# Kernel tuning notes

Hardware: AMD Instinct MI355X
Metric: run time of the kernel (lower is better)

The kernel has to match this reference:

```python
import jax, jax.numpy as jnp
import numpy as np

K = 16

def _pairwise_distance(points):
    # points: (B, N, F) -> (B, N, N)
    r = jnp.sum(points * points, axis=2, keepdims=True)  # (B,N,1)
    m = jnp.einsum('bnf,bmf->bnm', points, points)
    return r - 2.0 * m + jnp.swapaxes(r, 1, 2) + 1e-5

def _block(points, features, W1, b1, W2, b2):
    D = _pairwise_distance(points)
    _, idx = jax.lax.top_k(-D, K + 1)          # (B,N,K+1)
    idx = idx[:, :, 1:]                          # drop self -> (B,N,K)
    neighbors = jax.vmap(lambda f, i: f[i])(features, idx)  # (B,N,K,C)
    center = jnp.broadcast_to(features[:, :, None, :], neighbors.shape)
    edge = jnp.concatenate([neighbors - center, center], axis=-1)  # (B,N,K,2C)
    h = jax.nn.gelu(edge @ W1 + b1, approximate=False)
    h = jax.nn.gelu(h @ W2 + b2, approximate=False)
    return jnp.mean(h, axis=2)  # (B,N,proj)

def setup_inputs() -> dict:
    key = jax.random.key(0)
    ks = jax.random.split(key, 8)
    B, N, C_in, P, F = 64, 512, 32, 64, 3
    s = lambda fan: 1.0 / np.sqrt(fan)
    return {
        'x': jax.random.normal(ks[0], (B, N, C_in), jnp.float32),
        'points': jax.random.normal(ks[1], (B, N, F), jnp.float32),
        'mask': jax.random.randint(ks[2], (B, N, 1), 0, 2).astype(jnp.int32),
        'W1_0': jax.random.normal(ks[3], (2 * C_in, 2 * P), jnp.float32) * s(2 * C_in),
        'b1_0': jnp.zeros((2 * P,), jnp.float32),
        'W2_0': jax.random.normal(ks[4], (2 * P, P), jnp.float32) * s(2 * P),
        'b2_0': jnp.zeros((P,), jnp.float32),
        'W1_1': jax.random.normal(ks[5], (2 * P, 2 * P), jnp.float32) * s(2 * P),
        'b1_1': jnp.zeros((2 * P,), jnp.float32),
        'W2_1': jax.random.normal(ks[6], (2 * P, P), jnp.float32) * s(2 * P),
        'b2_1': jnp.zeros((P,), jnp.float32),
    }

def reference(x, points, mask, W1_0, b1_0, W2_0, b2_0, W1_1, b1_1, W2_1, b2_1):
    mask_f = mask.astype(jnp.float32)
    coord_shift = 999.0 * (mask == 0).astype(jnp.float32)  # (B,N,1)
    feats = _block(coord_shift + points, x, W1_0, b1_0, W2_0, b2_0)
    feats = _block(coord_shift + feats, feats, W1_1, b1_1, W2_1, b2_1)
    return feats * mask_f
```

## Files before the change

kernel.cpp:

```cpp
#include <hip/hip_runtime.h>
#include <math.h>

#define BB 64
#define NN 512
#define KK 16

__device__ __forceinline__ float gelu32(float x) {
    return 0.5f * x * (1.0f + erff(x * 0.70710678118654752440f));
}

#define TAB_N 521
__device__ __forceinline__ double gelu64_tab(double x, const double2* s_tab) {
    double ax = fabs(x);
    if (ax >= 5.74) return x > 0.0 ? x : 0.0;
    double z = ax * 0.70710678118654752440;
    double u = z * 128.0;
    int i = (int)(u + 0.5);
    double zi = (double)i * (1.0 / 128.0);
    double d = z - zi;
    double2 t = s_tab[i];
    double poly = d * (1.0 + d * (-zi + d * ((2.0 * zi * zi - 1.0) * (1.0 / 3.0))));
    double er = t.x + t.y * poly;
    double s = (x > 0.0) ? er : -er;
    return 0.5 * x * (1.0 + s);
}

__global__ void build_tab(double2* __restrict__ g_tab) {
    for (int i = threadIdx.x; i < TAB_N; i += 256) {
        double z = (double)i * (1.0 / 128.0);
        double2 e;
        e.x = erf(z);
        e.y = 1.12837916709551257390 * exp(-z * z);
        g_tab[i] = e;
    }
}

#define SELECT_TOP17(d, lane, OUT_STMT)                                        \
    for (int it = 0; it <= KK; ++it) {                                         \
        double bd = d[0];                                                      \
        int bi = lane;                                                         \
        _Pragma("unroll")                                                      \
        for (int i = 1; i < 8; ++i) {                                          \
            int m = lane + 64 * i;                                             \
            if (d[i] < bd) { bd = d[i]; bi = m; }                              \
        }                                                                      \
        for (int off = 32; off > 0; off >>= 1) {                               \
            double od = __shfl_xor(bd, off, 64);                               \
            int    oi = __shfl_xor(bi, off, 64);                               \
            if (od < bd || (od == bd && oi < bi)) { bd = od; bi = oi; }        \
        }                                                                      \
        const int wl = bi & 63, wsl = bi >> 6;                                 \
        _Pragma("unroll")                                                      \
        for (int i = 0; i < 8; ++i)                                            \
            if (lane == wl && i == wsl) d[i] = 1e300;                          \
        if (it > 0 && lane == 0) { OUT_STMT; }                                 \
    }

__global__ __launch_bounds__(512) void knn1_uv1(const float* __restrict__ points,
                                                const int* __restrict__ mask,
                                                const float* __restrict__ x,
                                                const float* __restrict__ W1,
                                                int* __restrict__ idx_out,
                                                double* __restrict__ U1) {
    __shared__ double sbuf[3 * NN];
    const int tid = threadIdx.x;

    if (blockIdx.x < BB * NN / 8) {
        double (*pts)[NN] = (double (*)[NN])sbuf;
        const int b = blockIdx.x >> 6;
        const int n0 = (blockIdx.x & 63) * 8;
        const int w = tid >> 6, lane = tid & 63;

        for (int e = tid; e < NN; e += 512) {
            double sh = (mask[b * NN + e] == 0) ? 999.0 : 0.0;
            const float* p = points + ((size_t)b * NN + e) * 3;
            pts[0][e] = (double)p[0] + sh;
            pts[1][e] = (double)p[1] + sh;
            pts[2][e] = (double)p[2] + sh;
        }
        __syncthreads();

        const int n = n0 + w;
        if (mask[b * NN + n] == 0) return;
        const double q0 = pts[0][n], q1 = pts[1][n], q2 = pts[2][n];
        double d[8];
        #pragma unroll
        for (int i = 0; i < 8; ++i) {
            int m = lane + 64 * i;
            double d0 = q0 - pts[0][m], d1 = q1 - pts[1][m], d2 = q2 - pts[2][m];
            d[i] = d0 * d0 + d1 * d1 + d2 * d2;
        }

        int* orow = idx_out + (size_t)(b * NN + n) * KK;
        SELECT_TOP17(d, lane, orow[it - 1] = bi)
    } else {
        double (*xs)[32] = (double (*)[32])sbuf;
        const int row0 = (blockIdx.x - BB * NN / 8) * 8;
        if (tid < 256) xs[tid >> 5][tid & 31] = (double)x[(size_t)row0 * 32 + tid];
        __syncthreads();
        const int j = tid & 127;
        const int rr = tid >> 7;
        #pragma unroll
        for (int p = 0; p < 2; ++p) {
            const int r = p * 4 + rr;
            const int row = row0 + r;
            if (mask[row] != 0) {
                double acc = 0.0;
                #pragma unroll 4
                for (int c = 0; c < 32; ++c) acc += xs[r][c] * (double)W1[c * 128 + j];
                U1[(size_t)row * 128 + j] = acc;
            }
        }
    }
}

template<int UV>
__global__ __launch_bounds__(256, 2) void mlp1_f64(const float* __restrict__ x,
                                                   const int* __restrict__ idx,
                                                   const float* __restrict__ W1,
                                                   const float* __restrict__ b1,
                                                   const float* __restrict__ W2,
                                                   const float* __restrict__ b2,
                                                   const float* __restrict__ W1n,
                                                   const double2* __restrict__ g_tab,
                                                   const int* __restrict__ mask,
                                                   const double* __restrict__ U1,
                                                   double* __restrict__ feats_out,
                                                   double* __restrict__ rm,
                                                   double* __restrict__ Sq,
                                                   float* __restrict__ U2) {
    const int C = 32;
    __shared__ double2 s_tab[TAB_N];
    __shared__ double ctr[32];
    __shared__ double H1[KK][128];
    __shared__ double part[4][64];
    __shared__ float f_row[64];
    const int swz = ((blockIdx.x & 7) << 12) + (blockIdx.x >> 3);
    const int b = swz >> 9;
    const int bn = swz;
    const int tid = threadIdx.x;

    if (mask[bn] == 0) {
        if (tid == 0) { rm[bn] = 1e18; Sq[bn] = 0.0; }
        return;
    }

    for (int i = tid; i < TAB_N; i += 256) s_tab[i] = g_tab[i];
    if (tid < C) ctr[tid] = (double)x[(size_t)bn * C + tid];
    __syncthreads();

    if constexpr (UV) {
        const int j = tid & 127;
        const int kb = (tid >> 7) * 8;
        double tn = (double)b1[j];
        #pragma unroll 4
        for (int c = 0; c < C; ++c)
            tn += ctr[c] * ((double)W1[(C + c) * 128 + j] - (double)W1[c * 128 + j]);
        #pragma unroll
        for (int kk = 0; kk < 8; ++kk) {
            int m = idx[bn * KK + kb + kk];
            double v = U1[(size_t)(b * NN + m) * 128 + j] + tn;
            H1[kb + kk][j] = gelu64_tab(v, s_tab);
        }
    } else {
        __shared__ double edg[KK][32];
        for (int e = tid; e < KK * C; e += 256) {
            int k = e >> 5, c = e & 31;
            int m = idx[bn * KK + k];
            edg[k][c] = (double)x[((size_t)b * NN + m) * C + c] - ctr[c];
        }
        __syncthreads();
        const int j = tid & 127;
        const int kb = (tid >> 7) * 8;
        double cterm = (double)b1[j];
        #pragma unroll 2
        for (int c = 0; c < C; ++c) cterm += ctr[c] * (double)W1[(C + c) * 128 + j];
        double acc[8];
        #pragma unroll
        for (int kk = 0; kk < 8; ++kk) acc[kk] = cterm;
        #pragma unroll 2
        for (int c = 0; c < C; ++c) {
            double w = (double)W1[c * 128 + j];
            #pragma unroll
            for (int kk = 0; kk < 8; ++kk) acc[kk] += edg[kb + kk][c] * w;
        }
        #pragma unroll
        for (int kk = 0; kk < 8; ++kk) H1[kb + kk][j] = gelu64_tab(acc[kk], s_tab);
    }
    __syncthreads();

    {
        const int j = tid & 63;
        const int g = tid >> 6;
        const int kb = g * 4;
        double acc[4];
        #pragma unroll
        for (int kk = 0; kk < 4; ++kk) acc[kk] = (double)b2[j];
        #pragma unroll 4
        for (int c = 0; c < 128; ++c) {
            double w = (double)W2[c * 64 + j];
            #pragma unroll
            for (int kk = 0; kk < 4; ++kk) acc[kk] += H1[kb + kk][c] * w;
        }
        double s = 0.0;
        #pragma unroll
        for (int kk = 0; kk < 4; ++kk) s += gelu64_tab(acc[kk], s_tab);
        part[g][j] = s;
    }
    __syncthreads();

    if (tid < 64) {
        double s = (part[0][tid] + part[1][tid] + part[2][tid] + part[3][tid]) * 0.0625;
        feats_out[(size_t)bn * 64 + tid] = s;
        f_row[tid] = (float)s;
        double s2 = s * s, s1 = s;
        for (int off = 32; off > 0; off >>= 1) {
            s2 += __shfl_xor(s2, off, 64);
            s1 += __shfl_xor(s1, off, 64);
        }
        if (tid == 0) { rm[bn] = s2; Sq[bn] = s1; }
    }
    if constexpr (UV) {
        __syncthreads();
        if (tid < 128) {
            float acc = 0.0f;
            #pragma unroll 4
            for (int c = 0; c < 64; ++c) acc += f_row[c] * W1n[c * 128 + tid];
            U2[(size_t)bn * 128 + tid] = acc;
        }
    }
}

__global__ __launch_bounds__(512) void knn2(const double* __restrict__ feats,
                                            const int* __restrict__ mask,
                                            const double* __restrict__ rm,
                                            const double* __restrict__ Sq,
                                            int* __restrict__ idx_out) {
    __shared__ double tileT[64][65];
    __shared__ double qsh[8][64];
    __shared__ double qrn[8], qSq[8];
    const int bid = ((blockIdx.x & 7) << 9) + (blockIdx.x >> 3);
    const int b = bid >> 6;
    const int n0 = (bid & 63) * 8;
    const int tid = threadIdx.x;
    const int w = tid >> 6, lane = tid & 63;
    const int n = n0 + w;
    const int qm = mask[b * NN + n];

    {
        qsh[w][lane] = feats[(size_t)(b * NN + n) * 64 + lane];
        if (lane == 0) { qrn[w] = rm[b * NN + n]; qSq[w] = Sq[b * NN + n]; }
    }
    __syncthreads();

    double d[8];
    #pragma unroll
    for (int t = 0; t < 8; ++t) {
        #pragma unroll
        for (int i = 0; i < 8; ++i) {
            int e = tid + 512 * i;
            int f = e & 63, c = e >> 6;
            tileT[f][c] = feats[(size_t)(b * NN + t * 64 + c) * 64 + f];
        }
        __syncthreads();
        if (qm) {
            int m = t * 64 + lane;
            double sh_m = (mask[b * NN + m] == 0) ? 999.0 : 0.0;
            double a0 = 0.0, a1 = 0.0, a2 = 0.0, a3 = 0.0;
            for (int f = 0; f < 64; f += 4) {
                a0 += qsh[w][f + 0] * tileT[f + 0][lane];
                a1 += qsh[w][f + 1] * tileT[f + 1][lane];
                a2 += qsh[w][f + 2] * tileT[f + 2][lane];
                a3 += qsh[w][f + 3] * tileT[f + 3][lane];
            }
            double dot = (a0 + a1) + (a2 + a3);
            d[t] = qrn[w] + rm[b * NN + m] - 2.0 * (dot + sh_m * qSq[w]) + 1e-5;
        }
        __syncthreads();
    }

    if (qm) {
        int* orow = idx_out + (size_t)(b * NN + n) * KK;
        SELECT_TOP17(d, lane, orow[it - 1] = bi)
    }
}

template<int UV>
__global__ __launch_bounds__(256, 2) void mlp2_f32(const double* __restrict__ feats,
                                                   const int* __restrict__ idx,
                                                   const float* __restrict__ W1,
                                                   const float* __restrict__ b1,
                                                   const float* __restrict__ W2,
                                                   const float* __restrict__ b2,
                                                   const int* __restrict__ mask,
                                                   const float* __restrict__ U2,
                                                   float* __restrict__ out) {
    const int C = 64;
    __shared__ float ctr[64];
    __shared__ float H1[KK][128];
    __shared__ float part[4][64];
    const int swz = ((blockIdx.x & 7) << 12) + (blockIdx.x >> 3);
    const int b = swz >> 9;
    const int bn = swz;
    const int tid = threadIdx.x;

    if (mask[bn] == 0) {
        if (tid < 64) out[(size_t)bn * 64 + tid] = 0.0f;
        return;
    }

    if (tid < C) ctr[tid] = (float)feats[(size_t)bn * C + tid];
    __syncthreads();

    if constexpr (UV) {
        const int j = tid & 127;
        const int kb = (tid >> 7) * 8;
        float tn = b1[j];
        #pragma unroll 4
        for (int c = 0; c < C; ++c)
            tn += ctr[c] * (W1[(C + c) * 128 + j] - W1[c * 128 + j]);
        #pragma unroll
        for (int kk = 0; kk < 8; ++kk) {
            int m = idx[bn * KK + kb + kk];
            H1[kb + kk][j] = gelu32(U2[(size_t)(b * NN + m) * 128 + j] + tn);
        }
    } else {
        __shared__ float edg[KK][64];
        for (int e = tid; e < KK * C; e += 256) {
            int k = e >> 6, c = e & 63;
            int m = idx[bn * KK + k];
            edg[k][c] = (float)feats[((size_t)b * NN + m) * C + c] - ctr[c];
        }
        __syncthreads();
        const int j = tid & 127;
        const int kb = (tid >> 7) * 8;
        float cterm = b1[j];
        #pragma unroll 2
        for (int c = 0; c < C; ++c) cterm += ctr[c] * W1[(C + c) * 128 + j];
        float acc[8];
        #pragma unroll
        for (int kk = 0; kk < 8; ++kk) acc[kk] = cterm;
        #pragma unroll 2
        for (int c = 0; c < C; ++c) {
            float w = W1[c * 128 + j];
            #pragma unroll
            for (int kk = 0; kk < 8; ++kk) acc[kk] += edg[kb + kk][c] * w;
        }
        #pragma unroll
        for (int kk = 0; kk < 8; ++kk) H1[kb + kk][j] = gelu32(acc[kk]);
    }
    __syncthreads();

    {
        const int j = tid & 63;
        const int g = tid >> 6;
        const int kb = g * 4;
        float acc[4];
        #pragma unroll
        for (int kk = 0; kk < 4; ++kk) acc[kk] = b2[j];
        #pragma unroll 4
        for (int c = 0; c < 128; ++c) {
            float w = W2[c * 64 + j];
            #pragma unroll
            for (int kk = 0; kk < 4; ++kk) acc[kk] += H1[kb + kk][c] * w;
        }
        float s = 0.0f;
        #pragma unroll
        for (int kk = 0; kk < 4; ++kk) s += gelu32(acc[kk]);
        part[g][j] = s;
    }
    __syncthreads();

    if (tid < 64) {
        float s = (part[0][tid] + part[1][tid] + part[2][tid] + part[3][tid]) * 0.0625f;
        out[(size_t)bn * 64 + tid] = s;
    }
}

extern "C" void kernel_launch(void* const* d_in, const int* in_sizes, int n_in,
                              void* d_out, int out_size, void* d_ws, size_t ws_size,
                              hipStream_t stream) {
    const float* x      = (const float*)d_in[0];
    const float* points = (const float*)d_in[1];
    const int*   mask   = (const int*)d_in[2];
    const float* W1_0 = (const float*)d_in[3];
    const float* b1_0 = (const float*)d_in[4];
    const float* W2_0 = (const float*)d_in[5];
    const float* b2_0 = (const float*)d_in[6];
    const float* W1_1 = (const float*)d_in[7];
    const float* b1_1 = (const float*)d_in[8];
    const float* W2_1 = (const float*)d_in[9];
    const float* b2_1 = (const float*)d_in[10];

    char* ws = (char*)d_ws;
    const size_t off_tab   = 0;
    const size_t off_idx   = 16384;
    const size_t off_feats = off_idx + 2097152;
    const size_t off_rm    = off_feats + 16777216;
    const size_t off_sq    = off_rm + 262144;
    const size_t off_u1    = off_sq + 262144;
    const size_t off_u2    = off_u1 + 33554432;
    const size_t need      = off_u2 + 16777216;

    double2* tab    = (double2*)(ws + off_tab);
    int*     idx    = (int*)(ws + off_idx);
    double*  feats1 = (double*)(ws + off_feats);
    double*  rm     = (double*)(ws + off_rm);
    double*  Sq     = (double*)(ws + off_sq);
    double*  U1     = (double*)(ws + off_u1);
    float*   U2     = (float*)(ws + off_u2);

    const int use_uv = (ws_size >= need) ? 1 : 0;
    const int knn1_blocks = BB * NN / 8;
    const int grid1 = knn1_blocks + (use_uv ? BB * NN / 8 : 0);

    build_tab<<<1, 256, 0, stream>>>(tab);
    knn1_uv1<<<grid1, 512, 0, stream>>>(points, mask, x, W1_0, idx, U1);
    if (use_uv) {
        mlp1_f64<1><<<BB * NN, 256, 0, stream>>>(x, idx, W1_0, b1_0, W2_0, b2_0, W1_1,
                                                 tab, mask, U1, feats1, rm, Sq, U2);
        knn2<<<BB * NN / 8, 512, 0, stream>>>(feats1, mask, rm, Sq, idx);
        mlp2_f32<1><<<BB * NN, 256, 0, stream>>>(feats1, idx, W1_1, b1_1, W2_1, b2_1,
                                                 mask, U2, (float*)d_out);
    } else {
        mlp1_f64<0><<<BB * NN, 256, 0, stream>>>(x, idx, W1_0, b1_0, W2_0, b2_0, W1_1,
                                                 tab, mask, U1, feats1, rm, Sq, U2);
        knn2<<<BB * NN / 8, 512, 0, stream>>>(feats1, mask, rm, Sq, idx);
        mlp2_f32<0><<<BB * NN, 256, 0, stream>>>(feats1, idx, W1_1, b1_1, W2_1, b2_1,
                                                 mask, U2, (float*)d_out);
    }
}
```

Baseline: 698.8 us.

## Compact unmasked points per batch so second kNN skips masked candidates

Adds a per-batch stream compaction (ballot plus prefix) of unmasked point indices into the first kernel. The second kNN then only loads and scores unmasked candidates, mapping the selected slots back through the compacted list, and drops the Sq/shift term. Masked candidates sit 999 away, so they only matter when a batch has fewer than 17 valid points, which is an edge-case risk. Also halves the erf table resolution and vectorises the W2 LDS reads in both MLP kernels.

```diff
diff --git a/kernel.cpp b/kernel.cpp
--- a/kernel.cpp
+++ b/kernel.cpp
@@ -9,14 +9,14 @@
     return 0.5f * x * (1.0f + erff(x * 0.70710678118654752440f));
 }
 
-#define TAB_N 521
+#define TAB_N 261
 __device__ __forceinline__ double gelu64_tab(double x, const double2* s_tab) {
     double ax = fabs(x);
     if (ax >= 5.74) return x > 0.0 ? x : 0.0;
     double z = ax * 0.70710678118654752440;
-    double u = z * 128.0;
+    double u = z * 64.0;
     int i = (int)(u + 0.5);
-    double zi = (double)i * (1.0 / 128.0);
+    double zi = (double)i * (1.0 / 64.0);
     double d = z - zi;
     double2 t = s_tab[i];
     double poly = d * (1.0 + d * (-zi + d * ((2.0 * zi * zi - 1.0) * (1.0 / 3.0))));
@@ -27,7 +27,7 @@
 
 __global__ void build_tab(double2* __restrict__ g_tab) {
     for (int i = threadIdx.x; i < TAB_N; i += 256) {
-        double z = (double)i * (1.0 / 128.0);
+        double z = (double)i * (1.0 / 64.0);
         double2 e;
         e.x = erf(z);
         e.y = 1.12837916709551257390 * exp(-z * z);
@@ -60,8 +60,11 @@
                                                 const int* __restrict__ mask,
                                                 const float* __restrict__ x,
                                                 const float* __restrict__ W1,
+                                                int uvb,
                                                 int* __restrict__ idx_out,
-                                                double* __restrict__ U1) {
+                                                double* __restrict__ U1,
+                                                int* __restrict__ cu,
+                                                int* __restrict__ nU) {
     __shared__ double sbuf[3 * NN];
     const int tid = threadIdx.x;
 
@@ -93,7 +96,7 @@
 
         int* orow = idx_out + (size_t)(b * NN + n) * KK;
         SELECT_TOP17(d, lane, orow[it - 1] = bi)
-    } else {
+    } else if (blockIdx.x < BB * NN / 8 + uvb) {
         double (*xs)[32] = (double (*)[32])sbuf;
         const int row0 = (blockIdx.x - BB * NN / 8) * 8;
         if (tid < 256) xs[tid >> 5][tid & 31] = (double)x[(size_t)row0 * 32 + tid];
@@ -111,6 +114,23 @@
                 U1[(size_t)row * 128 + j] = acc;
             }
         }
+    } else {
+        __shared__ int wcnt[8], woff[8];
+        const int b = blockIdx.x - (BB * NN / 8 + uvb);
+        const int w = tid >> 6, lane = tid & 63;
+        const int bit = (mask[b * NN + tid] != 0) ? 1 : 0;
+        unsigned long long bal = __ballot(bit);
+        int pos = __popcll(bal & ((1ull << lane) - 1ull));
+        if (lane == 0) wcnt[w] = __popcll(bal);
+        __syncthreads();
+        if (tid == 0) {
+            int acc = 0;
+            #pragma unroll
+            for (int i = 0; i < 8; ++i) { woff[i] = acc; acc += wcnt[i]; }
+            nU[b] = acc;
+        }
+        __syncthreads();
+        if (bit) cu[b * NN + woff[w] + pos] = tid;
     }
 }
 
@@ -127,7 +147,6 @@
                                                    const double* __restrict__ U1,
                                                    double* __restrict__ feats_out,
                                                    double* __restrict__ rm,
-                                                   double* __restrict__ Sq,
                                                    float* __restrict__ U2) {
     const int C = 32;
     __shared__ double2 s_tab[TAB_N];
@@ -140,10 +159,7 @@
     const int bn = swz;
     const int tid = threadIdx.x;
 
-    if (mask[bn] == 0) {
-        if (tid == 0) { rm[bn] = 1e18; Sq[bn] = 0.0; }
-        return;
-    }
+    if (mask[bn] == 0) return;
 
     for (int i = tid; i < TAB_N; i += 256) s_tab[i] = g_tab[i];
     if (tid < C) ctr[tid] = (double)x[(size_t)bn * C + tid];
@@ -196,11 +212,18 @@
         double acc[4];
         #pragma unroll
         for (int kk = 0; kk < 4; ++kk) acc[kk] = (double)b2[j];
-        #pragma unroll 4
-        for (int c = 0; c < 128; ++c) {
-            double w = (double)W2[c * 64 + j];
-            #pragma unroll
-            for (int kk = 0; kk < 4; ++kk) acc[kk] += H1[kb + kk][c] * w;
+        #pragma unroll 2
+        for (int c = 0; c < 128; c += 2) {
+            double w0 = (double)W2[c * 64 + j];
+            double w1 = (double)W2[(c + 1) * 64 + j];
+            double2 h0 = *(const double2*)&H1[kb + 0][c];
+            double2 h1 = *(const double2*)&H1[kb + 1][c];
+            double2 h2 = *(const double2*)&H1[kb + 2][c];
+            double2 h3 = *(const double2*)&H1[kb + 3][c];
+            acc[0] += h0.x * w0; acc[0] += h0.y * w1;
+            acc[1] += h1.x * w0; acc[1] += h1.y * w1;
+            acc[2] += h2.x * w0; acc[2] += h2.y * w1;
+            acc[3] += h3.x * w0; acc[3] += h3.y * w1;
         }
         double s = 0.0;
         #pragma unroll
@@ -213,12 +236,9 @@
         double s = (part[0][tid] + part[1][tid] + part[2][tid] + part[3][tid]) * 0.0625;
         feats_out[(size_t)bn * 64 + tid] = s;
         f_row[tid] = (float)s;
-        double s2 = s * s, s1 = s;
-        for (int off = 32; off > 0; off >>= 1) {
-            s2 += __shfl_xor(s2, off, 64);
-            s1 += __shfl_xor(s1, off, 64);
-        }
-        if (tid == 0) { rm[bn] = s2; Sq[bn] = s1; }
+        double s2 = s * s;
+        for (int off = 32; off > 0; off >>= 1) s2 += __shfl_xor(s2, off, 64);
+        if (tid == 0) rm[bn] = s2;
     }
     if constexpr (UV) {
         __syncthreads();
@@ -234,11 +254,14 @@
 __global__ __launch_bounds__(512) void knn2(const double* __restrict__ feats,
                                             const int* __restrict__ mask,
                                             const double* __restrict__ rm,
-                                            const double* __restrict__ Sq,
+                                            const int* __restrict__ cu,
+                                            const int* __restrict__ nU,
                                             int* __restrict__ idx_out) {
     __shared__ double tileT[64][65];
     __shared__ double qsh[8][64];
-    __shared__ double qrn[8], qSq[8];
+    __shared__ double qrn[8];
+    __shared__ int cI[NN];
+    __shared__ int s_nU;
     const int bid = ((blockIdx.x & 7) << 9) + (blockIdx.x >> 3);
     const int b = bid >> 6;
     const int n0 = (bid & 63) * 8;
@@ -247,41 +270,48 @@
     const int n = n0 + w;
     const int qm = mask[b * NN + n];
 
-    {
-        qsh[w][lane] = feats[(size_t)(b * NN + n) * 64 + lane];
-        if (lane == 0) { qrn[w] = rm[b * NN + n]; qSq[w] = Sq[b * NN + n]; }
-    }
-    __syncthreads();
+    if (tid == 0) s_nU = nU[b];
+    for (int e = tid; e < NN; e += 512) cI[e] = cu[b * NN + e];
+    qsh[w][lane] = feats[(size_t)(b * NN + n) * 64 + lane];
+    if (lane == 0) qrn[w] = rm[b * NN + n];
+    __syncthreads();
+
+    const int nUl = s_nU;
+    const int ntiles = (nUl + 63) >> 6;
 
     double d[8];
     #pragma unroll
     for (int t = 0; t < 8; ++t) {
-        #pragma unroll
-        for (int i = 0; i < 8; ++i) {
-            int e = tid + 512 * i;
-            int f = e & 63, c = e >> 6;
-            tileT[f][c] = feats[(size_t)(b * NN + t * 64 + c) * 64 + f];
-        }
-        __syncthreads();
-        if (qm) {
-            int m = t * 64 + lane;
-            double sh_m = (mask[b * NN + m] == 0) ? 999.0 : 0.0;
-            double a0 = 0.0, a1 = 0.0, a2 = 0.0, a3 = 0.0;
-            for (int f = 0; f < 64; f += 4) {
-                a0 += qsh[w][f + 0] * tileT[f + 0][lane];
-                a1 += qsh[w][f + 1] * tileT[f + 1][lane];
-                a2 += qsh[w][f + 2] * tileT[f + 2][lane];
-                a3 += qsh[w][f + 3] * tileT[f + 3][lane];
+        d[t] = 1e300;
+        if (t < ntiles) {
+            #pragma unroll
+            for (int i = 0; i < 8; ++i) {
+                int e = tid + 512 * i;
+                int f = e & 63, c = e >> 6;
+                int slot = t * 64 + c;
+                if (slot < nUl)
+                    tileT[f][c] = feats[(size_t)(b * NN + cI[slot]) * 64 + f];
             }
-            double dot = (a0 + a1) + (a2 + a3);
-            d[t] = qrn[w] + rm[b * NN + m] - 2.0 * (dot + sh_m * qSq[w]) + 1e-5;
-        }
-        __syncthreads();
+            __syncthreads();
+            int slot = t * 64 + lane;
+            if (qm && slot < nUl) {
+                double a0 = 0.0, a1 = 0.0, a2 = 0.0, a3 = 0.0;
+                for (int f = 0; f < 64; f += 4) {
+                    a0 += qsh[w][f + 0] * tileT[f + 0][lane];
+                    a1 += qsh[w][f + 1] * tileT[f + 1][lane];
+                    a2 += qsh[w][f + 2] * tileT[f + 2][lane];
+                    a3 += qsh[w][f + 3] * tileT[f + 3][lane];
+                }
+                double dot = (a0 + a1) + (a2 + a3);
+                d[t] = qrn[w] + rm[b * NN + cI[slot]] - 2.0 * dot + 1e-5;
+            }
+            __syncthreads();
+        }
     }
 
     if (qm) {
         int* orow = idx_out + (size_t)(b * NN + n) * KK;
-        SELECT_TOP17(d, lane, orow[it - 1] = bi)
+        SELECT_TOP17(d, lane, orow[it - 1] = cI[bi])
     }
 }
 
@@ -358,11 +388,18 @@
         float acc[4];
         #pragma unroll
         for (int kk = 0; kk < 4; ++kk) acc[kk] = b2[j];
-        #pragma unroll 4
-        for (int c = 0; c < 128; ++c) {
-            float w = W2[c * 64 + j];
+        #pragma unroll 2
+        for (int c = 0; c < 128; c += 4) {
+            float w0 = W2[(c + 0) * 64 + j];
+            float w1 = W2[(c + 1) * 64 + j];
+            float w2 = W2[(c + 2) * 64 + j];
+            float w3 = W2[(c + 3) * 64 + j];
             #pragma unroll
-            for (int kk = 0; kk < 4; ++kk) acc[kk] += H1[kb + kk][c] * w;
+            for (int kk = 0; kk < 4; ++kk) {
+                float4 h = *(const float4*)&H1[kb + kk][c];
+                acc[kk] += h.x * w0; acc[kk] += h.y * w1;
+                acc[kk] += h.z * w2; acc[kk] += h.w * w3;
+            }
         }
         float s = 0.0f;
         #pragma unroll
@@ -397,8 +434,9 @@
     const size_t off_idx   = 16384;
     const size_t off_feats = off_idx + 2097152;
     const size_t off_rm    = off_feats + 16777216;
-    const size_t off_sq    = off_rm + 262144;
-    const size_t off_u1    = off_sq + 262144;
+    const size_t off_cu    = off_rm + 262144;
+    const size_t off_nu    = off_cu + 131072;
+    const size_t off_u1    = off_nu + 4096;
     const size_t off_u2    = off_u1 + 33554432;
     const size_t need      = off_u2 + 16777216;
 
@@ -406,26 +444,27 @@
     int*     idx    = (int*)(ws + off_idx);
     double*  feats1 = (double*)(ws + off_feats);
     double*  rm     = (double*)(ws + off_rm);
-    double*  Sq     = (double*)(ws + off_sq);
+    int*     cu     = (int*)(ws + off_cu);
+    int*     nU     = (int*)(ws + off_nu);
     double*  U1     = (double*)(ws + off_u1);
     float*   U2     = (float*)(ws + off_u2);
 
     const int use_uv = (ws_size >= need) ? 1 : 0;
-    const int knn1_blocks = BB * NN / 8;
-    const int grid1 = knn1_blocks + (use_uv ? BB * NN / 8 : 0);
+    const int uvb = use_uv ? BB * NN / 8 : 0;
+    const int grid1 = BB * NN / 8 + uvb + BB;
 
     build_tab<<<1, 256, 0, stream>>>(tab);
-    knn1_uv1<<<grid1, 512, 0, stream>>>(points, mask, x, W1_0, idx, U1);
+    knn1_uv1<<<grid1, 512, 0, stream>>>(points, mask, x, W1_0, uvb, idx, U1, cu, nU);
     if (use_uv) {
         mlp1_f64<1><<<BB * NN, 256, 0, stream>>>(x, idx, W1_0, b1_0, W2_0, b2_0, W1_1,
-                                                 tab, mask, U1, feats1, rm, Sq, U2);
-        knn2<<<BB * NN / 8, 512, 0, stream>>>(feats1, mask, rm, Sq, idx);
+                                                 tab, mask, U1, feats1, rm, U2);
+        knn2<<<BB * NN / 8, 512, 0, stream>>>(feats1, mask, rm, cu, nU, idx);
         mlp2_f32<1><<<BB * NN, 256, 0, stream>>>(feats1, idx, W1_1, b1_1, W2_1, b2_1,
                                                  mask, U2, (float*)d_out);
     } else {
         mlp1_f64<0><<<BB * NN, 256, 0, stream>>>(x, idx, W1_0, b1_0, W2_0, b2_0, W1_1,
-                                                 tab, mask, U1, feats1, rm, Sq, U2);
-        knn2<<<BB * NN / 8, 512, 0, stream>>>(feats1, mask, rm, Sq, idx);
+                                                 tab, mask, U1, feats1, rm, U2);
+        knn2<<<BB * NN / 8, 512, 0, stream>>>(feats1, mask, rm, cu, nU, idx);
         mlp2_f32<0><<<BB * NN, 256, 0, stream>>>(feats1, idx, W1_1, b1_1, W2_1, b2_1,
                                                  mask, U2, (float*)d_out);
     }
```

New measurement: 644.2 us. 7.8% less time.
